# Kernel tuning notes

Hardware: AMD Instinct MI355X
Metric: run time of the kernel (lower is better)

Reference implementation:

```python
import jax, jax.numpy as jnp
import numpy as np

B, L, E, H = 4, 2048, 1024, 16
D = E // H  # head_dim = 64

def setup_inputs() -> dict:
    key = jax.random.key(0)
    ks = jax.random.split(key, 8)
    s = 1.0 / np.sqrt(E)
    return {
        "x_q": jax.random.normal(ks[0], (B, L, E), jnp.float32),
        "x_k": jax.random.normal(ks[1], (B, L, E), jnp.float32),
        "x_v": jax.random.normal(ks[2], (B, L, E), jnp.float32),
        "Wq": jax.random.uniform(ks[3], (E, E), jnp.float32, -s, s),
        "Wk": jax.random.uniform(ks[4], (E, E), jnp.float32, -s, s),
        "Wv": jax.random.uniform(ks[5], (E, E), jnp.float32, -s, s),
        "Wo": jax.random.uniform(ks[6], (E, E), jnp.float32, -s, s),
        "bo": jax.random.uniform(ks[7], (E,), jnp.float32, -s, s),
    }

def reference(x_q, x_k, x_v, Wq, Wk, Wv, Wo, bo):
    # projections (torch Linear: y = x @ W.T)
    Q = (x_q @ Wq.T).reshape(B, L, H, D).transpose(0, 2, 1, 3)  # (B,H,Lq,D)
    K = (x_k @ Wk.T).reshape(B, L, H, D).transpose(0, 2, 1, 3)
    V = (x_v @ Wv.T).reshape(B, L, H, D).transpose(0, 2, 1, 3)
    scale = 1.0 / jnp.sqrt(jnp.asarray(D, Q.dtype))
    scores = jnp.einsum('bhqd,bhkd->bhqk', Q, K) * scale  # (B,H,Lq,Lk)
    attn = jax.nn.softmax(scores, axis=-1)
    ctx = jnp.einsum('bhqk,bhkd->bhqd', attn, V)
    ctx = ctx.transpose(0, 2, 1, 3).reshape(B, L, E)
    return ctx @ Wo.T + bo
```

## Files before the change

kernel.cpp:

```cpp
#include <hip/hip_runtime.h>
#include <hip/hip_bf16.h>
#include <stdint.h>

typedef __bf16 bf16;
typedef __attribute__((ext_vector_type(8))) __bf16 bf16x8;
typedef __attribute__((ext_vector_type(4))) __bf16 bf16x4;
typedef __attribute__((ext_vector_type(4))) float f32x4;
typedef __attribute__((ext_vector_type(16))) float f32x16;
typedef __attribute__((ext_vector_type(4))) unsigned int u32x4;

#define MFMA(a, b, c) __builtin_amdgcn_mfma_f32_16x16x32_bf16(a, b, c, 0, 0, 0)
#define MFMA32(a, b, c) __builtin_amdgcn_mfma_f32_32x32x16_bf16(a, b, c, 0, 0, 0)

__device__ __forceinline__ void gload16(const void* g, void* l) {
  __builtin_amdgcn_global_load_lds(
      (const __attribute__((address_space(1))) void*)g,
      (__attribute__((address_space(3))) void*)l, 16, 0, 0);
}

__global__ void cvt4(const float* __restrict__ s0, const float* __restrict__ s1,
                     const float* __restrict__ s2, const float* __restrict__ s3,
                     bf16* __restrict__ d0, bf16* __restrict__ d1,
                     bf16* __restrict__ d2, bf16* __restrict__ d3, long n) {
  const float* s = blockIdx.y == 0 ? s0 : blockIdx.y == 1 ? s1 : blockIdx.y == 2 ? s2 : s3;
  bf16* d       = blockIdx.y == 0 ? d0 : blockIdx.y == 1 ? d1 : blockIdx.y == 2 ? d2 : d3;
  long i0 = ((long)blockIdx.x * blockDim.x + threadIdx.x) * 8;
  long gs = (long)gridDim.x * blockDim.x * 8;
  for (long i = i0; i < n; i += gs) {
    float4 a = *(const float4*)(s + i);
    float4 b = *(const float4*)(s + i + 4);
    bf16x8 ov;
    ov[0] = (bf16)a.x; ov[1] = (bf16)a.y; ov[2] = (bf16)a.z; ov[3] = (bf16)a.w;
    ov[4] = (bf16)b.x; ov[5] = (bf16)b.y; ov[6] = (bf16)b.z; ov[7] = (bf16)b.w;
    *(bf16x8*)(d + i) = ov;
  }
}

__device__ __forceinline__ void gemm_epilogue(f32x4 (&acc)[4][4], void* Cout,
                                              const float* bias, float scale,
                                              int mode, int m0, int n0, int wm,
                                              int wn, int lr, int lg) {
  for (int i = 0; i < 4; i++)
    for (int j = 0; j < 4; j++) {
      int row = m0 + wm * 64 + i * 16 + lg * 4;
      int col = n0 + wn * 64 + j * 16 + lr;
      f32x4 v = acc[i][j];
      if (mode == 2) {
        float* O = (float*)Cout;
        float bb = bias[col];
        for (int r = 0; r < 4; r++) O[(long)(row + r) * 1024 + col] = v[r] + bb;
      } else if (mode == 0) {
        bf16* O = (bf16*)Cout;
        for (int r = 0; r < 4; r++) {
          int rr = row + r;
          long idx = ((long)((rr >> 11) * 16 + (col >> 6)) * 2048 + (rr & 2047)) * 64 + (col & 63);
          O[idx] = (bf16)(v[r] * scale);
        }
      } else {
        bf16* O = (bf16*)Cout;
        long idx = ((long)((row >> 11) * 16 + (col >> 6)) * 64 + (col & 63)) * 2048 + (row & 2047);
        bf16x4 pk;
        for (int r = 0; r < 4; r++) pk[r] = (bf16)v[r];
        *(bf16x4*)(O + idx) = pk;
      }
    }
}

__global__ __launch_bounds__(256) void gemm_qkv(const float* __restrict__ xq,
                                                const float* __restrict__ xk,
                                                const float* __restrict__ xv,
                                                const bf16* __restrict__ Wb,
                                                bf16* __restrict__ Ob,
                                                float qscale) {
  __shared__ float As[3][128 * 32];
  __shared__ bf16 Bs[3][128 * 32];
  const int z = blockIdx.z;
  const float* A = z == 0 ? xq : (z == 1 ? xk : xv);
  const bf16* W = Wb + (long)z * 1024 * 1024;
  bf16* O = Ob + (long)z * 8192 * 1024;
  const float scale = (z == 0) ? qscale : 1.0f;
  const int mode = (z == 2) ? 1 : 0;

  const int tid = threadIdx.x;
  const int l = tid & 63, w = tid >> 6;
  const int lr = l & 15, lg = l >> 4;
  const int lin = blockIdx.y * 8 + blockIdx.x;
  const int nl = (lin & 7) * 64 + (lin >> 3);
  const int m0 = (nl >> 3) * 128, n0 = (nl & 7) * 128;
  const int wm = w >> 1, wn = w & 1;
  f32x4 acc[4][4];
  for (int i = 0; i < 4; i++)
    for (int j = 0; j < 4; j++)
      for (int r = 0; r < 4; r++) acc[i][j][r] = 0.f;

  auto STAGE = [&](int kt, int buf) {
#pragma unroll
    for (int i = 0; i < 4; i++) {
      int c = i * 256 + tid;
      int row = c >> 3, ch = c & 7;
      int g = ch ^ (row & 7);
      gload16(A + (long)(m0 + row) * 1024 + kt + g * 4, (char*)As[buf] + c * 16);
    }
#pragma unroll
    for (int i = 0; i < 2; i++) {
      int c = i * 256 + tid;
      int row = c >> 2, ch = c & 3;
      int g = ch ^ ((row >> 1) & 3);
      gload16(W + (long)(n0 + row) * 1024 + kt + g * 8, (char*)Bs[buf] + c * 16);
    }
  };

  STAGE(0, 0);
  STAGE(32, 1);

  for (int t = 0; t < 32; t++) {
    if (t < 31) asm volatile("s_waitcnt vmcnt(6) lgkmcnt(0)" ::: "memory");
    else        asm volatile("s_waitcnt vmcnt(0) lgkmcnt(0)" ::: "memory");
    __builtin_amdgcn_s_barrier();
    __builtin_amdgcn_sched_barrier(0);
    const int rb = t % 3;
    const char* Ac = (const char*)As[rb];
    const char* Bc = (const char*)Bs[rb];
    bf16x8 af[4], bw[4];
#pragma unroll
    for (int i = 0; i < 4; i++) {
      int row = wm * 64 + i * 16 + lr;
      const char* base = Ac + row * 128;
      f32x4 lo = *(const f32x4*)(base + (((2 * lg) ^ (row & 7)) << 4));
      f32x4 hi = *(const f32x4*)(base + (((2 * lg + 1) ^ (row & 7)) << 4));
      bf16x8 v;
      v[0] = (bf16)lo[0]; v[1] = (bf16)lo[1]; v[2] = (bf16)lo[2]; v[3] = (bf16)lo[3];
      v[4] = (bf16)hi[0]; v[5] = (bf16)hi[1]; v[6] = (bf16)hi[2]; v[7] = (bf16)hi[3];
      af[i] = v;
    }
#pragma unroll
    for (int j = 0; j < 4; j++) {
      int row = wn * 64 + j * 16 + lr;
      bw[j] = *(const bf16x8*)(Bc + row * 64 + ((lg ^ ((row >> 1) & 3)) << 4));
    }
#pragma unroll
    for (int i = 0; i < 4; i++)
#pragma unroll
      for (int j = 0; j < 4; j++)
        acc[i][j] = MFMA(af[i], bw[j], acc[i][j]);
    if (t <= 29) STAGE((t + 2) * 32, (t + 2) % 3);
  }

  gemm_epilogue(acc, O, nullptr, scale, mode, m0, n0, wm, wn, lr, lg);
}

__global__ __launch_bounds__(256) void gemm_out(const bf16* __restrict__ A,
                                                const bf16* __restrict__ W,
                                                float* __restrict__ Cout,
                                                const float* __restrict__ bias) {
  __shared__ bf16 As[4][128 * 32];
  __shared__ bf16 Bs[4][128 * 32];
  const int tid = threadIdx.x;
  const int l = tid & 63, w = tid >> 6;
  const int lr = l & 15, lg = l >> 4;
  const int lin = blockIdx.y * 8 + blockIdx.x;
  const int nl = (lin & 7) * 64 + (lin >> 3);
  const int m0 = (nl >> 3) * 128, n0 = (nl & 7) * 128;
  const int wm = w >> 1, wn = w & 1;
  f32x4 acc[4][4];
  for (int i = 0; i < 4; i++)
    for (int j = 0; j < 4; j++)
      for (int r = 0; r < 4; r++) acc[i][j][r] = 0.f;

  auto STAGE = [&](int kt, int buf) {
#pragma unroll
    for (int i = 0; i < 2; i++) {
      int c = i * 256 + tid;
      int row = c >> 2, ch = c & 3;
      int sc = (ch ^ ((row >> 1) & 3)) * 8;
      gload16(A + (long)(m0 + row) * 1024 + kt + sc, (char*)As[0] + buf * 8192 + c * 16);
      gload16(W + (long)(n0 + row) * 1024 + kt + sc, (char*)Bs[0] + buf * 8192 + c * 16);
    }
  };

  STAGE(0, 0); STAGE(32, 1); STAGE(64, 2);

  for (int t = 0; t < 32; t++) {
    if (t <= 29)      asm volatile("s_waitcnt vmcnt(8) lgkmcnt(0)" ::: "memory");
    else if (t == 30) asm volatile("s_waitcnt vmcnt(4) lgkmcnt(0)" ::: "memory");
    else              asm volatile("s_waitcnt vmcnt(0) lgkmcnt(0)" ::: "memory");
    __builtin_amdgcn_s_barrier();
    __builtin_amdgcn_sched_barrier(0);
    const char* Ac = (const char*)As[0] + (t & 3) * 8192;
    const char* Bc = (const char*)Bs[0] + (t & 3) * 8192;
    bf16x8 af[4], bw[4];
#pragma unroll
    for (int i = 0; i < 4; i++) {
      int row = wm * 64 + i * 16 + lr;
      af[i] = *(const bf16x8*)(Ac + row * 64 + ((lg ^ ((row >> 1) & 3)) << 4));
    }
#pragma unroll
    for (int j = 0; j < 4; j++) {
      int row = wn * 64 + j * 16 + lr;
      bw[j] = *(const bf16x8*)(Bc + row * 64 + ((lg ^ ((row >> 1) & 3)) << 4));
    }
#pragma unroll
    for (int i = 0; i < 4; i++)
#pragma unroll
      for (int j = 0; j < 4; j++)
        acc[i][j] = MFMA(af[i], bw[j], acc[i][j]);
    if (t <= 28) STAGE((t + 3) * 32, (t + 3) & 3);
  }

  gemm_epilogue(acc, Cout, bias, 1.0f, 2, m0, n0, wm, wn, lr, lg);
}

__global__ __launch_bounds__(512, 4) void attn_fwd(const bf16* __restrict__ Q,
                                                   const bf16* __restrict__ K,
                                                   const bf16* __restrict__ Vt,
                                                   bf16* __restrict__ ctx) {
  __shared__ bf16 Ks[2][128 * 64];
  __shared__ bf16 Vs[2][64 * 128];
  const int tid = threadIdx.x;
  const int l = tid & 63, w = tid >> 6;
  const int q32 = l & 31, hl = l >> 5;
  const int lin = blockIdx.y * 8 + blockIdx.x;
  const int nl = (lin & 7) * 64 + (lin >> 3);
  const int bh = nl >> 3, qt = nl & 7;
  const bf16* Qh = Q + (long)bh * 2048 * 64;
  const bf16* Kh = K + (long)bh * 2048 * 64;
  const bf16* Vh = Vt + (long)bh * 64 * 2048;
  const int qb = qt * 256 + w * 32;

#define STAGE(kv0, buf)                                                          \
  {                                                                              \
    _Pragma("unroll") for (int i = 0; i < 2; i++) {                              \
      int c = i * 512 + tid;                                                     \
      int kr = c >> 3, kc = c & 7;                                               \
      gload16(Kh + (long)((kv0) + kr) * 64 + ((kc ^ (kr & 7)) << 3),             \
              (char*)Ks[buf] + c * 16);                                          \
    }                                                                            \
    _Pragma("unroll") for (int i = 0; i < 2; i++) {                              \
      int c = i * 512 + tid;                                                     \
      int r = c >> 4, v0 = c & 15;                                               \
      int vc = (v0 & 8) | ((v0 & 7) ^ (r & 7));                                  \
      gload16(Vh + (long)r * 2048 + (kv0) + vc * 8,                              \
              (char*)Vs[buf] + c * 16);                                          \
    }                                                                            \
  }

  bf16x8 bq[4];
#pragma unroll
  for (int kk = 0; kk < 4; kk++)
    bq[kk] = *(const bf16x8*)(Qh + (long)(qb + q32) * 64 + kk * 16 + hl * 8);

  f32x16 o0, o1;
#pragma unroll
  for (int r = 0; r < 16; r++) { o0[r] = 0.f; o1[r] = 0.f; }
  float lrun = 0.f;

  STAGE(0, 0);
  __syncthreads();

  for (int t = 0; t < 16; t++) {
    const int cur = t & 1;
    if (t < 15) STAGE((t + 1) * 128, cur ^ 1);
    const bf16* Kc = Ks[cur];
    const bf16* Vc = Vs[cur];
    f32x4 psum = {0.f, 0.f, 0.f, 0.f};

#pragma unroll
    for (int nn = 0; nn < 4; nn++) {
      const int row = nn * 32 + q32;
      f32x16 acc;
#pragma unroll
      for (int r = 0; r < 16; r++) acc[r] = 0.f;
      __builtin_amdgcn_s_setprio(1);
#pragma unroll
      for (int kk = 0; kk < 4; kk++) {
        int ch = (kk * 2 + hl) ^ (row & 7);
        bf16x8 ak = *(const bf16x8*)((const char*)Kc + row * 128 + (ch << 4));
        acc = MFMA32(ak, bq[kk], acc);
      }
      __builtin_amdgcn_s_setprio(0);

      f32x16 p;
#pragma unroll
      for (int r = 0; r < 16; r++) p[r] = __builtin_amdgcn_exp2f(acc[r]);
      f32x4 t4;
#pragma unroll
      for (int j = 0; j < 4; j++) t4[j] = (p[j] + p[4 + j]) + (p[8 + j] + p[12 + j]);
      psum += t4;

      unsigned wd[8];
#pragma unroll
      for (int i = 0; i < 8; i++) {
        float lo = p[2 * i], hi = p[2 * i + 1];
        asm("v_cvt_pk_bf16_f32 %0, %1, %2" : "=v"(wd[i]) : "v"(lo), "v"(hi));
      }
#pragma unroll
      for (int ss = 0; ss < 2; ss++) {
        unsigned a0 = wd[ss * 4 + 0], b0 = wd[ss * 4 + 2];
        unsigned a1 = wd[ss * 4 + 1], b1 = wd[ss * 4 + 3];
        asm("v_permlane32_swap_b32 %0, %1" : "+v"(a0), "+v"(b0));
        asm("v_permlane32_swap_b32 %0, %1" : "+v"(a1), "+v"(b1));
        u32x4 pw = {a0, a1, b0, b1};
        bf16x8 bp = *(bf16x8*)&pw;
        int ch0 = (nn * 2 + ss) * 2 + hl;
        __builtin_amdgcn_s_setprio(1);
#pragma unroll
        for (int nd = 0; nd < 2; nd++) {
          int vrw = nd * 32 + q32;
          int ch = (ch0 & 8) | ((ch0 & 7) ^ (vrw & 7));
          bf16x8 av = *(const bf16x8*)((const char*)Vc + vrw * 256 + (ch << 4));
          if (nd == 0) o0 = MFMA32(av, bp, o0);
          else         o1 = MFMA32(av, bp, o1);
        }
        __builtin_amdgcn_s_setprio(0);
      }
    }
    lrun += (psum[0] + psum[1]) + (psum[2] + psum[3]);
    __syncthreads();
  }

  lrun += __shfl_xor(lrun, 32);
  const int b = bh >> 4, h = bh & 15;
  const float inv = 1.0f / lrun;
  const int q = qb + q32;
#pragma unroll
  for (int nd = 0; nd < 2; nd++)
#pragma unroll
    for (int qd = 0; qd < 4; qd++) {
      bf16x4 pk;
#pragma unroll
      for (int r = 0; r < 4; r++)
        pk[r] = (bf16)((nd == 0 ? o0[qd * 4 + r] : o1[qd * 4 + r]) * inv);
      int d = nd * 32 + qd * 8 + hl * 4;
      *(bf16x4*)(ctx + ((long)b * 2048 + q) * 1024 + h * 64 + d) = pk;
    }
#undef STAGE
}

extern "C" void kernel_launch(void* const* d_in, const int* in_sizes, int n_in,
                              void* d_out, int out_size, void* d_ws, size_t ws_size,
                              hipStream_t stream) {
  const float* xq = (const float*)d_in[0];
  const float* xk = (const float*)d_in[1];
  const float* xv = (const float*)d_in[2];
  const float* Wq = (const float*)d_in[3];
  const float* Wk = (const float*)d_in[4];
  const float* Wv = (const float*)d_in[5];
  const float* Wo = (const float*)d_in[6];
  const float* bo = (const float*)d_in[7];

  char* p = (char*)d_ws;
  const size_t SZ_X = (size_t)8192 * 1024 * 2;
  const size_t SZ_W = (size_t)1024 * 1024 * 2;
  bf16* wqb = (bf16*)p; p += SZ_W;
  bf16* wkb = (bf16*)p; p += SZ_W;
  bf16* wvb = (bf16*)p; p += SZ_W;
  bf16* wob = (bf16*)p; p += SZ_W;
  bf16* Qb  = (bf16*)p; p += SZ_X;
  bf16* Kb  = (bf16*)p; p += SZ_X;
  bf16* Vtb = (bf16*)p; p += SZ_X;
  bf16* ctxb = (bf16*)p; p += SZ_X;
  (void)ws_size; (void)in_sizes; (void)n_in; (void)out_size;

  const float QSCALE = 0.18033688011112042f;

  cvt4<<<dim3(128, 4), 256, 0, stream>>>(Wq, Wk, Wv, Wo, wqb, wkb, wvb, wob,
                                         (long)1024 * 1024);
  gemm_qkv<<<dim3(8, 64, 3), 256, 0, stream>>>(xq, xk, xv, wqb, Qb, QSCALE);
  attn_fwd<<<dim3(8, 64), 512, 0, stream>>>(Qb, Kb, Vtb, ctxb);
  gemm_out<<<dim3(8, 64), 256, 0, stream>>>(ctxb, wob, (float*)d_out, bo);
}
```

Before: 193.8 us.

## Split attention KV range across two blocks and merge partials in combine kernel

Attention now splits the key/value sequence into two halves via a third grid dimension. Each block handles 1024 keys with smaller 64-key LDS tiles and writes unnormalized fp32 partial outputs and row sums to workspace. A new combine kernel adds the halves, normalizes, and transposes through LDS into the bf16 context layout. This doubles the block count to fill the GPU better and halves LDS per block. In exchange it adds fp32 partial-output traffic and an extra kernel launch. The merge needs no max rescale because the scores are not max-subtracted.

```diff
diff --git a/kernel.cpp b/kernel.cpp
--- a/kernel.cpp
+++ b/kernel.cpp
@@ -213,35 +213,29 @@
 __global__ __launch_bounds__(512, 4) void attn_fwd(const bf16* __restrict__ Q,
                                                    const bf16* __restrict__ K,
                                                    const bf16* __restrict__ Vt,
-                                                   bf16* __restrict__ ctx) {
-  __shared__ bf16 Ks[2][128 * 64];
-  __shared__ bf16 Vs[2][64 * 128];
+                                                   float* __restrict__ Opart,
+                                                   float* __restrict__ Lpart) {
+  __shared__ bf16 Ks[2][64 * 64];
+  __shared__ bf16 Vs[2][64 * 64];
   const int tid = threadIdx.x;
   const int l = tid & 63, w = tid >> 6;
   const int q32 = l & 31, hl = l >> 5;
+  const int half = blockIdx.z;
   const int lin = blockIdx.y * 8 + blockIdx.x;
   const int nl = (lin & 7) * 64 + (lin >> 3);
   const int bh = nl >> 3, qt = nl & 7;
   const bf16* Qh = Q + (long)bh * 2048 * 64;
-  const bf16* Kh = K + (long)bh * 2048 * 64;
-  const bf16* Vh = Vt + (long)bh * 64 * 2048;
+  const bf16* Kh = K + (long)bh * 2048 * 64 + (long)half * 1024 * 64;
+  const bf16* Vh = Vt + (long)bh * 64 * 2048 + half * 1024;
   const int qb = qt * 256 + w * 32;
+  const int sr = tid >> 3, sc = tid & 7;
 
 #define STAGE(kv0, buf)                                                          \
   {                                                                              \
-    _Pragma("unroll") for (int i = 0; i < 2; i++) {                              \
-      int c = i * 512 + tid;                                                     \
-      int kr = c >> 3, kc = c & 7;                                               \
-      gload16(Kh + (long)((kv0) + kr) * 64 + ((kc ^ (kr & 7)) << 3),             \
-              (char*)Ks[buf] + c * 16);                                          \
-    }                                                                            \
-    _Pragma("unroll") for (int i = 0; i < 2; i++) {                              \
-      int c = i * 512 + tid;                                                     \
-      int r = c >> 4, v0 = c & 15;                                               \
-      int vc = (v0 & 8) | ((v0 & 7) ^ (r & 7));                                  \
-      gload16(Vh + (long)r * 2048 + (kv0) + vc * 8,                              \
-              (char*)Vs[buf] + c * 16);                                          \
-    }                                                                            \
+    gload16(Kh + (long)((kv0) + sr) * 64 + ((sc ^ (sr & 7)) << 3),               \
+            (char*)Ks[buf] + tid * 16);                                          \
+    gload16(Vh + (long)sr * 2048 + (kv0) + ((sc ^ (sr & 7)) << 3),               \
+            (char*)Vs[buf] + tid * 16);                                          \
   }
 
   bf16x8 bq[4];
@@ -259,13 +253,13 @@
 
   for (int t = 0; t < 16; t++) {
     const int cur = t & 1;
-    if (t < 15) STAGE((t + 1) * 128, cur ^ 1);
+    if (t < 15) STAGE((t + 1) * 64, cur ^ 1);
     const bf16* Kc = Ks[cur];
     const bf16* Vc = Vs[cur];
     f32x4 psum = {0.f, 0.f, 0.f, 0.f};
 
 #pragma unroll
-    for (int nn = 0; nn < 4; nn++) {
+    for (int nn = 0; nn < 2; nn++) {
       const int row = nn * 32 + q32;
       f32x16 acc;
 #pragma unroll
@@ -273,7 +267,7 @@
       __builtin_amdgcn_s_setprio(1);
 #pragma unroll
       for (int kk = 0; kk < 4; kk++) {
-        int ch = (kk * 2 + hl) ^ (row & 7);
+        int ch = (kk * 2 + hl) ^ (q32 & 7);
         bf16x8 ak = *(const bf16x8*)((const char*)Kc + row * 128 + (ch << 4));
         acc = MFMA32(ak, bq[kk], acc);
       }
@@ -306,8 +300,8 @@
 #pragma unroll
         for (int nd = 0; nd < 2; nd++) {
           int vrw = nd * 32 + q32;
-          int ch = (ch0 & 8) | ((ch0 & 7) ^ (vrw & 7));
-          bf16x8 av = *(const bf16x8*)((const char*)Vc + vrw * 256 + (ch << 4));
+          int ch = ch0 ^ (q32 & 7);
+          bf16x8 av = *(const bf16x8*)((const char*)Vc + vrw * 128 + (ch << 4));
           if (nd == 0) o0 = MFMA32(av, bp, o0);
           else         o1 = MFMA32(av, bp, o1);
         }
@@ -319,21 +313,56 @@
   }
 
   lrun += __shfl_xor(lrun, 32);
+  float* Ob = Opart + ((long)(half * 64 + bh)) * 64 * 2048;
+#pragma unroll
+  for (int nd = 0; nd < 2; nd++)
+#pragma unroll
+    for (int qd = 0; qd < 4; qd++)
+#pragma unroll
+      for (int r = 0; r < 4; r++) {
+        int d = nd * 32 + qd * 8 + hl * 4 + r;
+        float v = (nd == 0) ? o0[qd * 4 + r] : o1[qd * 4 + r];
+        Ob[(long)d * 2048 + qb + q32] = v;
+      }
+  if (l < 32) Lpart[((long)half * 64 + bh) * 2048 + qb + q32] = lrun;
+#undef STAGE
+}
+
+__global__ __launch_bounds__(256) void combine(const float* __restrict__ Opart,
+                                               const float* __restrict__ Lpart,
+                                               bf16* __restrict__ ctx) {
+  __shared__ float invs[128];
+  __shared__ bf16 T[128][80];
+  const int bh = blockIdx.y, qt = blockIdx.x;
+  const int qb = qt * 128;
+  const int t = threadIdx.x;
+  const float* P0 = Opart + (long)bh * 64 * 2048;
+  const float* P1 = Opart + (long)(64 + bh) * 64 * 2048;
+  if (t < 128) {
+    float l0 = Lpart[(long)bh * 2048 + qb + t];
+    float l1 = Lpart[(long)(64 + bh) * 2048 + qb + t];
+    invs[t] = 1.0f / (l0 + l1);
+  }
+  __syncthreads();
+  const int r = t >> 2, cs = (t & 3) * 32;
+#pragma unroll
+  for (int i = 0; i < 8; i++) {
+    int qo = cs + i * 4;
+    f32x4 p0 = *(const f32x4*)(P0 + (long)r * 2048 + qb + qo);
+    f32x4 p1 = *(const f32x4*)(P1 + (long)r * 2048 + qb + qo);
+    f32x4 iv = *(const f32x4*)(&invs[qo]);
+#pragma unroll
+    for (int j = 0; j < 4; j++) T[qo + j][r] = (bf16)((p0[j] + p1[j]) * iv[j]);
+  }
+  __syncthreads();
   const int b = bh >> 4, h = bh & 15;
-  const float inv = 1.0f / lrun;
-  const int q = qb + q32;
-#pragma unroll
-  for (int nd = 0; nd < 2; nd++)
-#pragma unroll
-    for (int qd = 0; qd < 4; qd++) {
-      bf16x4 pk;
-#pragma unroll
-      for (int r = 0; r < 4; r++)
-        pk[r] = (bf16)((nd == 0 ? o0[qd * 4 + r] : o1[qd * 4 + r]) * inv);
-      int d = nd * 32 + qd * 8 + hl * 4;
-      *(bf16x4*)(ctx + ((long)b * 2048 + q) * 1024 + h * 64 + d) = pk;
-    }
-#undef STAGE
+#pragma unroll
+  for (int i = 0; i < 4; i++) {
+    int c = i * 256 + t;
+    int q = c >> 3, ch = c & 7;
+    bf16x8 v = *(const bf16x8*)(&T[q][ch * 8]);
+    *(bf16x8*)(ctx + ((long)b * 2048 + qb + q) * 1024 + h * 64 + ch * 8) = v;
+  }
 }
 
 extern "C" void kernel_launch(void* const* d_in, const int* in_sizes, int n_in,
@@ -359,6 +388,8 @@
   bf16* Kb  = (bf16*)p; p += SZ_X;
   bf16* Vtb = (bf16*)p; p += SZ_X;
   bf16* ctxb = (bf16*)p; p += SZ_X;
+  float* Opart = (float*)p; p += (size_t)2 * 64 * 64 * 2048 * 4;
+  float* Lpart = (float*)p; p += (size_t)2 * 64 * 2048 * 4;
   (void)ws_size; (void)in_sizes; (void)n_in; (void)out_size;
 
   const float QSCALE = 0.18033688011112042f;
@@ -366,6 +397,7 @@
   cvt4<<<dim3(128, 4), 256, 0, stream>>>(Wq, Wk, Wv, Wo, wqb, wkb, wvb, wob,
                                          (long)1024 * 1024);
   gemm_qkv<<<dim3(8, 64, 3), 256, 0, stream>>>(xq, xk, xv, wqb, Qb, QSCALE);
-  attn_fwd<<<dim3(8, 64), 512, 0, stream>>>(Qb, Kb, Vtb, ctxb);
+  attn_fwd<<<dim3(8, 64, 2), 512, 0, stream>>>(Qb, Kb, Vtb, Opart, Lpart);
+  combine<<<dim3(16, 64), 256, 0, stream>>>(Opart, Lpart, ctxb);
   gemm_out<<<dim3(8, 64), 256, 0, stream>>>(ctxb, wob, (float*)d_out, bo);
 }
```

Measured after the change: 230.0 us. 18.7% more time.

## Stage QKV activations through registers and store bf16 in LDS

Applied to the files above, without the earlier changes.

The QKV projection GEMM previously copied fp32 activation tiles straight into LDS by async global-to-LDS loads and converted them to bf16 on every fragment read. The new path loads the fp32 tile into registers, converts to bf16 once, and writes a smaller bf16 swizzled tile to LDS. That tile is written after the MFMAs for the next step, so the global loads overlap compute. This halves A-tile LDS footprint and read traffic and removes repeated per-wave conversions, at the cost of extra VGPRs for two register staging buffers and more complex vmcnt bookkeeping.

```diff
diff --git a/kernel.cpp b/kernel.cpp
--- a/kernel.cpp
+++ b/kernel.cpp
@@ -72,7 +72,7 @@
                                                 const bf16* __restrict__ Wb,
                                                 bf16* __restrict__ Ob,
                                                 float qscale) {
-  __shared__ float As[3][128 * 32];
+  __shared__ bf16 As[3][128 * 32];
   __shared__ bf16 Bs[3][128 * 32];
   const int z = blockIdx.z;
   const float* A = z == 0 ? xq : (z == 1 ? xk : xv);
@@ -93,14 +93,30 @@
     for (int j = 0; j < 4; j++)
       for (int r = 0; r < 4; r++) acc[i][j][r] = 0.f;
 
-  auto STAGE = [&](int kt, int buf) {
+  float4 ar0[4], ar1[4];
+
+  auto ALOAD = [&](int kt, float4* ar) {
 #pragma unroll
     for (int i = 0; i < 4; i++) {
       int c = i * 256 + tid;
-      int row = c >> 3, ch = c & 7;
-      int g = ch ^ (row & 7);
-      gload16(A + (long)(m0 + row) * 1024 + kt + g * 4, (char*)As[buf] + c * 16);
-    }
+      int row = c >> 3, fq = c & 7;
+      ar[i] = *(const float4*)(A + (long)(m0 + row) * 1024 + kt + fq * 4);
+    }
+  };
+  auto AWRITE = [&](const float4* ar, int buf) {
+#pragma unroll
+    for (int i = 0; i < 4; i++) {
+      int c = i * 256 + tid;
+      int row = c >> 3, fq = c & 7;
+      int g = fq >> 1;
+      bf16x4 pk;
+      pk[0] = (bf16)ar[i].x; pk[1] = (bf16)ar[i].y;
+      pk[2] = (bf16)ar[i].z; pk[3] = (bf16)ar[i].w;
+      *(bf16x4*)((char*)As[buf] + row * 64 + ((g ^ ((row >> 1) & 3)) << 4) +
+                 (fq & 1) * 8) = pk;
+    }
+  };
+  auto WSTAGE = [&](int kt, int buf) {
 #pragma unroll
     for (int i = 0; i < 2; i++) {
       int c = i * 256 + tid;
@@ -110,28 +126,29 @@
     }
   };
 
-  STAGE(0, 0);
-  STAGE(32, 1);
-
+  ALOAD(0, ar0); WSTAGE(0, 0);
+  ALOAD(32, ar1); WSTAGE(32, 1);
+  asm volatile("s_waitcnt vmcnt(6)" ::: "memory");
+  __builtin_amdgcn_sched_barrier(0);
+  AWRITE(ar0, 0);
+
+#pragma unroll 2
   for (int t = 0; t < 32; t++) {
-    if (t < 31) asm volatile("s_waitcnt vmcnt(6) lgkmcnt(0)" ::: "memory");
-    else        asm volatile("s_waitcnt vmcnt(0) lgkmcnt(0)" ::: "memory");
+    asm volatile("s_waitcnt lgkmcnt(0)" ::: "memory");
     __builtin_amdgcn_s_barrier();
     __builtin_amdgcn_sched_barrier(0);
-    const int rb = t % 3;
-    const char* Ac = (const char*)As[rb];
-    const char* Bc = (const char*)Bs[rb];
+    if (t <= 29) {
+      if ((t & 1) == 0) ALOAD((t + 2) * 32, ar0);
+      else              ALOAD((t + 2) * 32, ar1);
+      WSTAGE((t + 2) * 32, (t + 2) % 3);
+    }
+    const char* Ac = (const char*)As[t % 3];
+    const char* Bc = (const char*)Bs[t % 3];
     bf16x8 af[4], bw[4];
 #pragma unroll
     for (int i = 0; i < 4; i++) {
       int row = wm * 64 + i * 16 + lr;
-      const char* base = Ac + row * 128;
-      f32x4 lo = *(const f32x4*)(base + (((2 * lg) ^ (row & 7)) << 4));
-      f32x4 hi = *(const f32x4*)(base + (((2 * lg + 1) ^ (row & 7)) << 4));
-      bf16x8 v;
-      v[0] = (bf16)lo[0]; v[1] = (bf16)lo[1]; v[2] = (bf16)lo[2]; v[3] = (bf16)lo[3];
-      v[4] = (bf16)hi[0]; v[5] = (bf16)hi[1]; v[6] = (bf16)hi[2]; v[7] = (bf16)hi[3];
-      af[i] = v;
+      af[i] = *(const bf16x8*)(Ac + row * 64 + ((lg ^ ((row >> 1) & 3)) << 4));
     }
 #pragma unroll
     for (int j = 0; j < 4; j++) {
@@ -143,7 +160,13 @@
 #pragma unroll
       for (int j = 0; j < 4; j++)
         acc[i][j] = MFMA(af[i], bw[j], acc[i][j]);
-    if (t <= 29) STAGE((t + 2) * 32, (t + 2) % 3);
+    if (t <= 29)      asm volatile("s_waitcnt vmcnt(6)" ::: "memory");
+    else if (t == 30) asm volatile("s_waitcnt vmcnt(0)" ::: "memory");
+    __builtin_amdgcn_sched_barrier(0);
+    if (t <= 30) {
+      if ((t & 1) == 0) AWRITE(ar1, (t + 1) % 3);
+      else              AWRITE(ar0, (t + 1) % 3);
+    }
   }
 
   gemm_epilogue(acc, O, nullptr, scale, mode, m0, n0, wm, wn, lr, lg);
```

Result: faster. 189.4 us (-2.2%).
